# Optimization experiments

Hardware: AMD Instinct MI355X
Metric: run time of the kernel (lower is better)

## Reference

```python
import jax, jax.numpy as jnp
import numpy as np

T, E, H, K, WCNT, L = 131072, 512, 512, 1024, 50000, 128
NUM_LAYERS = 1


def setup_inputs() -> dict:
    key = jax.random.key(0)
    ks = jax.random.split(key, 12)
    f32 = jnp.float32
    return {
        "topic": jax.random.randint(ks[0], (L,), 0, WCNT, dtype=jnp.int32),
        "score_s": jax.random.uniform(ks[1], (1,), dtype=f32),
        "emb": jax.random.normal(ks[2], (WCNT, E), dtype=f32) * 0.05,
        "h": jax.random.normal(ks[3], (NUM_LAYERS, 1, H), dtype=f32) * 0.05,
        "vs": jax.random.normal(ks[4], (T, E), dtype=f32) * 0.05,
        "hs": jax.random.normal(ks[5], (T, 1, H), dtype=f32) * 0.05,
        "w_ih": jax.random.normal(ks[6], (3 * H, 2 * E + 1), dtype=f32) * 0.02,
        "w_hh": jax.random.normal(ks[7], (3 * H, H), dtype=f32) * 0.02,
        "b_ih": jnp.zeros((3 * H,), f32),
        "b_hh": jnp.zeros((3 * H,), f32),
        "w_score": jax.random.normal(ks[8], (1, E + 2 * H + 1), dtype=f32) * 0.02,
        "b_score": jnp.zeros((1,), f32),
    }


def _forward(topic, score_s, emb, h, vs, hs, w_ih, w_hh, b_ih, b_hh, w_score, b_score):
    # topic embedding: mean of word vectors -> v [E]
    v = emb[topic].mean(axis=0)
    # dot-product attention over growing history
    alpha = vs @ v                               # [T]
    vals, idx = jax.lax.top_k(alpha, K)          # top-k similar past items
    a = jax.nn.softmax(vals)                     # [K]
    hs_flat = hs.reshape(-1, NUM_LAYERS * H)     # [T, H]
    attn_h = a @ hs_flat[idx]                    # [H] weighted combine of gathered states
    length = jnp.full((1,), K, dtype=v.dtype)
    # with_last=True: cat([v, attn_h, h, length])
    pred_v = jnp.concatenate([v, attn_h, h.reshape(-1), length])[None, :]  # [1, E+2H+1]
    score = pred_v @ w_score.T + b_score         # [1, 1]
    # score_mode='double': split v by correctness of s
    pos = (score_s >= 0.5).astype(v.dtype)[0]
    x = jnp.concatenate([v * pos, v * (1.0 - pos), score_s])  # [2E+1]
    # single GRU step (torch gate layout: r, z, n)
    h_prev = h.reshape(H)
    gi = w_ih @ x + b_ih
    gh = w_hh @ h_prev + b_hh
    r = jax.nn.sigmoid(gi[:H] + gh[:H])
    z = jax.nn.sigmoid(gi[H:2 * H] + gh[H:2 * H])
    n = jnp.tanh(gi[2 * H:] + r * gh[2 * H:])
    h_new = ((1.0 - z) * n + z * h_prev).reshape(NUM_LAYERS, 1, H)
    # LSTMA updates the history
    vs_new = jnp.concatenate([vs, v[None, :]], axis=0)
    hs_new = jnp.concatenate([hs, h_new], axis=0)
    return score, h_new, vs_new, hs_new


def reference(topic, score_s, emb, h, vs, hs, w_ih, w_hh, b_ih, b_hh, w_score, b_score):
    return _forward(topic, score_s, emb, h, vs, hs, w_ih, w_hh, b_ih, b_hh, w_score, b_score)
```

## Files before the change

kernel.cpp:

```cpp
#include <hip/hip_runtime.h>
#include <math.h>

constexpr int T_ = 131072;
constexpr int E_ = 512;
constexpr int H_ = 512;
constexpr int K_ = 1024;
constexpr int L_ = 128;
constexpr int CAND_CAP = 16384;

typedef __attribute__((ext_vector_type(4))) float f32x4;

constexpr size_t OFF_V     = 0;
constexpr size_t OFF_ALPHA = 512;
constexpr size_t OFF_HIST1 = OFF_ALPHA + T_;
constexpr size_t OFF_CNT   = OFF_HIST1 + 65536;
constexpr size_t OFF_INFO  = OFF_CNT + 2;
constexpr size_t OFF_VALS  = OFF_INFO + 8;
constexpr size_t OFF_IDX   = OFF_VALS + K_;
constexpr size_t OFF_CANDV = OFF_IDX + K_;
constexpr size_t OFF_CANDI = OFF_CANDV + CAND_CAP;
constexpr size_t OFF_GI    = OFF_CANDI + CAND_CAP;
constexpr size_t OFF_GH    = OFF_GI + 3 * H_;

constexpr int ZERO_N = 65536 + 2;

constexpr size_t OUT_VS = 513;
constexpr size_t OUT_HS = 513 + (size_t)(T_ + 1) * E_;

constexpr int NB_GRU = 384;


__device__ __forceinline__ unsigned fkey(float f) {
    unsigned u = __float_as_uint(f);
    return (u & 0x80000000u) ? ~u : (u | 0x80000000u);
}

__global__ __launch_bounds__(1024) void k_init(const int* __restrict__ topic,
                                               const float* __restrict__ emb,
                                               float* __restrict__ ws_v,
                                               unsigned* __restrict__ zero_base,
                                               float* __restrict__ out) {
    if (blockIdx.x == gridDim.x - 1) {
        __shared__ float part[512];
        int t = threadIdx.x;
        int e = t & 511, g = t >> 9;
        float s = 0.f;
        #pragma unroll 8
        for (int l = g * 64; l < g * 64 + 64; ++l) {
            int tp = topic[l];
            s += emb[(size_t)tp * E_ + e];
        }
        if (g == 1) part[e] = s;
        __syncthreads();
        if (g == 0) {
            float v = (s + part[e]) * (1.0f / L_);
            ws_v[e] = v;
            out[OUT_VS + (size_t)T_ * E_ + e] = v;
        }
    } else {
        int i = blockIdx.x * blockDim.x + threadIdx.x;
        if (i < ZERO_N) zero_base[i] = 0u;
    }
}

__global__ __launch_bounds__(256) void k_mega(const float* __restrict__ vs,
                                              const float* __restrict__ hs,
                                              const float* __restrict__ ws_v,
                                              float* __restrict__ alpha,
                                              unsigned* __restrict__ hist1,
                                              const float* __restrict__ wih,
                                              const float* __restrict__ whh,
                                              const float* __restrict__ bih,
                                              const float* __restrict__ bhh,
                                              const float* __restrict__ score_s,
                                              const float* __restrict__ h_in,
                                              float* __restrict__ gi,
                                              float* __restrict__ gh,
                                              float* __restrict__ out) {
    __shared__ float x[1025 + 512];
    int t = threadIdx.x;
    int wave = t >> 6, lane = t & 63;
    int b = blockIdx.x;
    if (b < NB_GRU) {
        float ss = score_s[0];
        float pos = ss >= 0.5f ? 1.f : 0.f;
        for (int c = t; c < 1025; c += 256) {
            float xv;
            if (c < 512)       xv = ws_v[c] * pos;
            else if (c < 1024) xv = ws_v[c - 512] * (1.f - pos);
            else               xv = ss;
            x[c] = xv;
        }
        for (int c = t; c < 512; c += 256) x[1025 + c] = h_in[c];
        __syncthreads();
        int row = b * 4 + wave;
        const float* wr = wih + (size_t)row * 1025;
        float s1 = 0.f;
        for (int c = lane; c < 1025; c += 64) s1 = fmaf(wr[c], x[c], s1);
        const float* hr = whh + (size_t)row * 512;
        float s2 = 0.f;
        #pragma unroll
        for (int c = lane; c < 512; c += 64) s2 = fmaf(hr[c], x[1025 + c], s2);
        #pragma unroll
        for (int m = 32; m; m >>= 1) {
            s1 += __shfl_xor(s1, m, 64);
            s2 += __shfl_xor(s2, m, 64);
        }
        if (lane == 0) { gi[row] = s1 + bih[row]; gh[row] = s2 + bhh[row]; }
        return;
    }
    b -= NB_GRU;
    bool is_vs = b < (T_ / 4);
    int row = (is_vs ? b : b - T_ / 4) * 4 + wave;
    const f32x4* src4 = (const f32x4*)((is_vs ? vs : hs) + (size_t)row * E_);
    f32x4 a0 = __builtin_nontemporal_load(&src4[lane]);
    f32x4 a1 = __builtin_nontemporal_load(&src4[lane + 64]);
    if (is_vs) {
        const f32x4* v4 = (const f32x4*)ws_v;
        f32x4 b0 = v4[lane];
        f32x4 b1 = v4[lane + 64];
        float dot = 0.f;
        dot = fmaf(a0.x, b0.x, dot); dot = fmaf(a0.y, b0.y, dot);
        dot = fmaf(a0.z, b0.z, dot); dot = fmaf(a0.w, b0.w, dot);
        dot = fmaf(a1.x, b1.x, dot); dot = fmaf(a1.y, b1.y, dot);
        dot = fmaf(a1.z, b1.z, dot); dot = fmaf(a1.w, b1.w, dot);
        #pragma unroll
        for (int m = 32; m; m >>= 1) dot += __shfl_xor(dot, m, 64);
        if (lane == 0) {
            alpha[row] = dot;
            atomicAdd(&hist1[fkey(dot) >> 16], 1u);
        }
    }
    int nl = (lane + 1) & 63;
    float n0x = __shfl(a0.x, nl, 64), n0y = __shfl(a0.y, nl, 64), n0z = __shfl(a0.z, nl, 64);
    float n1x = __shfl(a1.x, nl, 64), n1y = __shfl(a1.y, nl, 64), n1z = __shfl(a1.z, nl, 64);
    float* dst = out + (is_vs ? OUT_VS : OUT_HS) + (size_t)row * E_;
    f32x4* d4 = (f32x4*)(dst + 3);
    bool last = (lane == 63);
    f32x4 lo;
    lo.x = a0.w;
    lo.y = last ? n1x : n0x;
    lo.z = last ? n1y : n0y;
    lo.w = last ? n1z : n0z;
    __builtin_nontemporal_store(lo, &d4[lane]);
    if (!last) {
        f32x4 hi;
        hi.x = a1.w; hi.y = n1x; hi.z = n1y; hi.w = n1z;
        __builtin_nontemporal_store(hi, &d4[lane + 64]);
    }
    if (lane == 0) { dst[0] = a0.x; dst[1] = a0.y; dst[2] = a0.z; }
    if (last) dst[511] = a1.w;
}

__global__ __launch_bounds__(256) void k_scan(const unsigned* __restrict__ hist,
                                              unsigned* __restrict__ info) {
    __shared__ unsigned ps[256];
    __shared__ unsigned s_chunk, s_above;
    int t = threadIdx.x;
    unsigned Kwant = (unsigned)K_;
    unsigned base = 65536u - (unsigned)(t + 1) * 256u;
    unsigned s = 0;
    for (int j = 0; j < 256; ++j) s += hist[base + j];
    ps[t] = s;
    __syncthreads();
    #pragma unroll
    for (int off = 1; off < 256; off <<= 1) {
        unsigned v = (t >= off) ? ps[t - off] : 0u;
        __syncthreads();
        ps[t] += v;
        __syncthreads();
    }
    unsigned incl = ps[t], excl = incl - s;
    if (excl < Kwant && incl >= Kwant) { s_chunk = (unsigned)t; s_above = excl; }
    __syncthreads();
    unsigned c = s_chunk;
    unsigned Kw2 = Kwant - s_above;
    unsigned bin = 65535u - c * 256u - (unsigned)t;
    unsigned b = hist[bin];
    __syncthreads();
    ps[t] = b;
    __syncthreads();
    #pragma unroll
    for (int off = 1; off < 256; off <<= 1) {
        unsigned v = (t >= off) ? ps[t - off] : 0u;
        __syncthreads();
        ps[t] += v;
        __syncthreads();
    }
    unsigned inc2 = ps[t], ex2 = inc2 - b;
    if (ex2 < Kw2 && inc2 >= Kw2) {
        info[0] = bin;
        info[1] = s_above + ex2;
    }
}

__global__ __launch_bounds__(256) void k_collect(const float* __restrict__ alpha,
                                                 const unsigned* __restrict__ info,
                                                 unsigned* __restrict__ cnt,
                                                 float* __restrict__ vals,
                                                 int* __restrict__ idx,
                                                 float* __restrict__ candv,
                                                 int* __restrict__ candi) {
    int i = blockIdx.x * blockDim.x + threadIdx.x;
    float a = alpha[i];
    unsigned hb = fkey(a) >> 16;
    unsigned bin1 = info[0];
    if (hb > bin1) {
        unsigned p = atomicAdd(&cnt[0], 1u);
        vals[p] = a; idx[p] = i;
    } else if (hb == bin1) {
        unsigned q = atomicAdd(&cnt[1], 1u);
        if (q < (unsigned)CAND_CAP) { candv[q] = a; candi[q] = i; }
    }
}

__global__ __launch_bounds__(256) void k_resolve(const float* __restrict__ candv,
                                                 const int* __restrict__ candi,
                                                 const unsigned* __restrict__ cnt,
                                                 float* __restrict__ vals,
                                                 int* __restrict__ idx) {
    int t = threadIdx.x;
    unsigned nc = cnt[1] < (unsigned)CAND_CAP ? cnt[1] : (unsigned)CAND_CAP;
    unsigned ndef = cnt[0];
    unsigned k2 = (unsigned)K_ - ndef;
    for (unsigned i = t; i < nc; i += 256) {
        unsigned ki = fkey(candv[i]);
        unsigned greater = 0, eqb = 0;
        for (unsigned j = 0; j < nc; ++j) {
            unsigned kj = fkey(candv[j]);
            greater += (kj > ki) ? 1u : 0u;
            eqb += (kj == ki && j < i) ? 1u : 0u;
        }
        unsigned r = greater + eqb;
        if (r < k2) { vals[ndef + r] = candv[i]; idx[ndef + r] = candi[i]; }
    }
}

__global__ __launch_bounds__(512) void k_attn(const float* __restrict__ hs,
                                              const float* __restrict__ vals,
                                              const int* __restrict__ idx,
                                              float* __restrict__ part) {
    __shared__ float red[512];
    int t = threadIdx.x, j = blockIdx.x;
    float v0 = vals[t], v1 = vals[t + 512];
    red[t] = fmaxf(v0, v1);
    __syncthreads();
    for (int s = 256; s > 0; s >>= 1) { if (t < s) red[t] = fmaxf(red[t], red[t + s]); __syncthreads(); }
    float m = red[0];
    __syncthreads();
    red[t] = expf(v0 - m) + expf(v1 - m);
    __syncthreads();
    for (int s = 256; s > 0; s >>= 1) { if (t < s) red[t] += red[t + s]; __syncthreads(); }
    float S = red[0];
    float acc = 0.f;
    #pragma unroll
    for (int k = j * 8; k < j * 8 + 8; ++k) {
        float w = expf(vals[k] - m) / S;
        acc = fmaf(w, hs[(size_t)idx[k] * E_ + t], acc);
    }
    part[(size_t)j * E_ + t] = acc;
}

__global__ __launch_bounds__(512) void k_final(const float* __restrict__ gi,
                                               const float* __restrict__ gh,
                                               const float* __restrict__ h_in,
                                               const float* __restrict__ part,
                                               const float* __restrict__ ws_v,
                                               const float* __restrict__ w_score,
                                               const float* __restrict__ b_score,
                                               float* __restrict__ out) {
    __shared__ float red[512];
    int j = threadIdx.x;
    float r = 1.f / (1.f + expf(-(gi[j] + gh[j])));
    float z = 1.f / (1.f + expf(-(gi[H_ + j] + gh[H_ + j])));
    float n = tanhf(gi[2 * H_ + j] + r * gh[2 * H_ + j]);
    float hp = h_in[j];
    float hn = (1.f - z) * n + z * hp;
    out[1 + j] = hn;
    out[OUT_HS + (size_t)T_ * E_ + j] = hn;
    float attn = 0.f;
    for (int jj = 0; jj < 128; ++jj) attn += part[(size_t)jj * E_ + j];
    float d = ws_v[j] * w_score[j] + attn * w_score[512 + j] + hp * w_score[1024 + j];
    if (j == 0) d += 1024.0f * w_score[1536] + b_score[0];
    red[j] = d;
    __syncthreads();
    for (int s = 256; s > 0; s >>= 1) { if (j < s) red[j] += red[j + s]; __syncthreads(); }
    if (j == 0) out[0] = red[0];
}

extern "C" void kernel_launch(void* const* d_in, const int* in_sizes, int n_in,
                              void* d_out, int out_size, void* d_ws, size_t ws_size,
                              hipStream_t stream) {
    const int*   topic   = (const int*)d_in[0];
    const float* score_s = (const float*)d_in[1];
    const float* emb     = (const float*)d_in[2];
    const float* h_in    = (const float*)d_in[3];
    const float* vs      = (const float*)d_in[4];
    const float* hs      = (const float*)d_in[5];
    const float* w_ih    = (const float*)d_in[6];
    const float* w_hh    = (const float*)d_in[7];
    const float* b_ih    = (const float*)d_in[8];
    const float* b_hh    = (const float*)d_in[9];
    const float* w_score = (const float*)d_in[10];
    const float* b_score = (const float*)d_in[11];
    float* out = (float*)d_out;

    float*    wsf   = (float*)d_ws;
    float*    v_ws  = wsf + OFF_V;
    float*    alpha = wsf + OFF_ALPHA;
    unsigned* hist1 = (unsigned*)(wsf + OFF_HIST1);
    unsigned* cnt   = (unsigned*)(wsf + OFF_CNT);
    unsigned* info  = (unsigned*)(wsf + OFF_INFO);
    float*    vals  = wsf + OFF_VALS;
    int*      idx   = (int*)(wsf + OFF_IDX);
    float*    candv = wsf + OFF_CANDV;
    int*      candi = (int*)(wsf + OFF_CANDI);
    float*    part  = wsf + OFF_ALPHA;
    float*    gi    = wsf + OFF_GI;
    float*    gh    = wsf + OFF_GH;

    hipLaunchKernelGGL(k_init, dim3(66), dim3(1024), 0, stream,
                       topic, emb, v_ws, hist1, out);
    hipLaunchKernelGGL(k_mega, dim3(NB_GRU + 2 * (T_ / 4)), dim3(256), 0, stream,
                       vs, hs, v_ws, alpha, hist1,
                       w_ih, w_hh, b_ih, b_hh, score_s, h_in, gi, gh, out);
    hipLaunchKernelGGL(k_scan, dim3(1), dim3(256), 0, stream, hist1, info);
    hipLaunchKernelGGL(k_collect, dim3(T_ / 256), dim3(256), 0, stream,
                       alpha, info, cnt, vals, idx, candv, candi);
    hipLaunchKernelGGL(k_resolve, dim3(1), dim3(256), 0, stream,
                       candv, candi, cnt, vals, idx);
    hipLaunchKernelGGL(k_attn, dim3(128), dim3(512), 0, stream, hs, vals, idx, part);
    hipLaunchKernelGGL(k_final, dim3(1), dim3(512), 0, stream,
                       gi, gh, h_in, part, v_ws, w_score, b_score, out);
}
```

Measured before the change: 227.6 us.

## Fold histogram scan into collect and merge attention with final scoring

The single-block scan kernel is removed. Every collect block now redundantly scans the 64K-bin histogram to find the threshold bin itself. The separate final kernel is also merged into the attention kernel: each attention block reduces its partial weighted state against the score weights and atomically adds into the output score, and an extra block does the GRU update. This drops two launches and the partial-sum buffer, at the cost of each of 512 collect blocks reading the full histogram and the score becoming an order-dependent atomic float sum.

```diff
diff --git a/kernel.cpp b/kernel.cpp
--- a/kernel.cpp
+++ b/kernel.cpp
@@ -10,12 +10,14 @@
 
 typedef __attribute__((ext_vector_type(4))) float f32x4;
 
+constexpr int NB_GRU = 384;
+constexpr unsigned NB_MEGA = NB_GRU + 2 * (T_ / 4);
+
 constexpr size_t OFF_V     = 0;
 constexpr size_t OFF_ALPHA = 512;
 constexpr size_t OFF_HIST1 = OFF_ALPHA + T_;
 constexpr size_t OFF_CNT   = OFF_HIST1 + 65536;
-constexpr size_t OFF_INFO  = OFF_CNT + 2;
-constexpr size_t OFF_VALS  = OFF_INFO + 8;
+constexpr size_t OFF_VALS  = OFF_CNT + 2;
 constexpr size_t OFF_IDX   = OFF_VALS + K_;
 constexpr size_t OFF_CANDV = OFF_IDX + K_;
 constexpr size_t OFF_CANDI = OFF_CANDV + CAND_CAP;
@@ -26,8 +28,6 @@
 
 constexpr size_t OUT_VS = 513;
 constexpr size_t OUT_HS = 513 + (size_t)(T_ + 1) * E_;
-
-constexpr int NB_GRU = 384;
 
 
 __device__ __forceinline__ unsigned fkey(float f) {
@@ -56,6 +56,7 @@
             float v = (s + part[e]) * (1.0f / L_);
             ws_v[e] = v;
             out[OUT_VS + (size_t)T_ * E_ + e] = v;
+            if (e == 0) out[0] = 0.f;
         }
     } else {
         int i = blockIdx.x * blockDim.x + threadIdx.x;
@@ -152,59 +153,51 @@
     if (last) dst[511] = a1.w;
 }
 
-__global__ __launch_bounds__(256) void k_scan(const unsigned* __restrict__ hist,
-                                              unsigned* __restrict__ info) {
-    __shared__ unsigned ps[256];
-    __shared__ unsigned s_chunk, s_above;
-    int t = threadIdx.x;
-    unsigned Kwant = (unsigned)K_;
-    unsigned base = 65536u - (unsigned)(t + 1) * 256u;
-    unsigned s = 0;
-    for (int j = 0; j < 256; ++j) s += hist[base + j];
-    ps[t] = s;
-    __syncthreads();
-    #pragma unroll
-    for (int off = 1; off < 256; off <<= 1) {
-        unsigned v = (t >= off) ? ps[t - off] : 0u;
-        __syncthreads();
-        ps[t] += v;
-        __syncthreads();
-    }
-    unsigned incl = ps[t], excl = incl - s;
-    if (excl < Kwant && incl >= Kwant) { s_chunk = (unsigned)t; s_above = excl; }
-    __syncthreads();
-    unsigned c = s_chunk;
-    unsigned Kw2 = Kwant - s_above;
-    unsigned bin = 65535u - c * 256u - (unsigned)t;
-    unsigned b = hist[bin];
-    __syncthreads();
-    ps[t] = b;
-    __syncthreads();
-    #pragma unroll
-    for (int off = 1; off < 256; off <<= 1) {
-        unsigned v = (t >= off) ? ps[t - off] : 0u;
-        __syncthreads();
-        ps[t] += v;
-        __syncthreads();
-    }
-    unsigned inc2 = ps[t], ex2 = inc2 - b;
-    if (ex2 < Kw2 && inc2 >= Kw2) {
-        info[0] = bin;
-        info[1] = s_above + ex2;
-    }
-}
-
 __global__ __launch_bounds__(256) void k_collect(const float* __restrict__ alpha,
-                                                 const unsigned* __restrict__ info,
+                                                 const unsigned* __restrict__ hist1,
                                                  unsigned* __restrict__ cnt,
                                                  float* __restrict__ vals,
                                                  int* __restrict__ idx,
                                                  float* __restrict__ candv,
                                                  int* __restrict__ candi) {
-    int i = blockIdx.x * blockDim.x + threadIdx.x;
+    __shared__ unsigned ps[258];
+    int t = threadIdx.x;
+    unsigned base = 65536u - (unsigned)(t + 1) * 256u;
+    unsigned s = 0;
+    for (int j = 0; j < 256; ++j) s += hist1[base + j];
+    ps[t] = s;
+    __syncthreads();
+    #pragma unroll
+    for (int off = 1; off < 256; off <<= 1) {
+        unsigned v = (t >= off) ? ps[t - off] : 0u;
+        __syncthreads();
+        ps[t] += v;
+        __syncthreads();
+    }
+    unsigned incl = ps[t], excl = incl - s;
+    if (excl < (unsigned)K_ && incl >= (unsigned)K_) { ps[256] = (unsigned)t; ps[257] = excl; }
+    __syncthreads();
+    unsigned c = ps[256];
+    unsigned Kw2 = (unsigned)K_ - ps[257];
+    unsigned bin = 65535u - c * 256u - (unsigned)t;
+    unsigned bv = hist1[bin];
+    __syncthreads();
+    ps[t] = bv;
+    __syncthreads();
+    #pragma unroll
+    for (int off = 1; off < 256; off <<= 1) {
+        unsigned v = (t >= off) ? ps[t - off] : 0u;
+        __syncthreads();
+        ps[t] += v;
+        __syncthreads();
+    }
+    unsigned inc2 = ps[t], ex2 = inc2 - bv;
+    if (ex2 < Kw2 && inc2 >= Kw2) ps[256] = bin;
+    __syncthreads();
+    unsigned bin1 = ps[256];
+    int i = blockIdx.x * 256 + t;
     float a = alpha[i];
     unsigned hb = fkey(a) >> 16;
-    unsigned bin1 = info[0];
     if (hb > bin1) {
         unsigned p = atomicAdd(&cnt[0], 1u);
         vals[p] = a; idx[p] = i;
@@ -239,53 +232,52 @@
 __global__ __launch_bounds__(512) void k_attn(const float* __restrict__ hs,
                                               const float* __restrict__ vals,
                                               const int* __restrict__ idx,
-                                              float* __restrict__ part) {
+                                              const float* __restrict__ gi,
+                                              const float* __restrict__ gh,
+                                              const float* __restrict__ h_in,
+                                              const float* __restrict__ ws_v,
+                                              const float* __restrict__ w_score,
+                                              const float* __restrict__ b_score,
+                                              float* __restrict__ out) {
     __shared__ float red[512];
     int t = threadIdx.x, j = blockIdx.x;
-    float v0 = vals[t], v1 = vals[t + 512];
-    red[t] = fmaxf(v0, v1);
-    __syncthreads();
-    for (int s = 256; s > 0; s >>= 1) { if (t < s) red[t] = fmaxf(red[t], red[t + s]); __syncthreads(); }
-    float m = red[0];
-    __syncthreads();
-    red[t] = expf(v0 - m) + expf(v1 - m);
-    __syncthreads();
-    for (int s = 256; s > 0; s >>= 1) { if (t < s) red[t] += red[t + s]; __syncthreads(); }
-    float S = red[0];
-    float acc = 0.f;
-    #pragma unroll
-    for (int k = j * 8; k < j * 8 + 8; ++k) {
-        float w = expf(vals[k] - m) / S;
-        acc = fmaf(w, hs[(size_t)idx[k] * E_ + t], acc);
-    }
-    part[(size_t)j * E_ + t] = acc;
-}
-
-__global__ __launch_bounds__(512) void k_final(const float* __restrict__ gi,
-                                               const float* __restrict__ gh,
-                                               const float* __restrict__ h_in,
-                                               const float* __restrict__ part,
-                                               const float* __restrict__ ws_v,
-                                               const float* __restrict__ w_score,
-                                               const float* __restrict__ b_score,
-                                               float* __restrict__ out) {
-    __shared__ float red[512];
-    int j = threadIdx.x;
-    float r = 1.f / (1.f + expf(-(gi[j] + gh[j])));
-    float z = 1.f / (1.f + expf(-(gi[H_ + j] + gh[H_ + j])));
-    float n = tanhf(gi[2 * H_ + j] + r * gh[2 * H_ + j]);
-    float hp = h_in[j];
-    float hn = (1.f - z) * n + z * hp;
-    out[1 + j] = hn;
-    out[OUT_HS + (size_t)T_ * E_ + j] = hn;
-    float attn = 0.f;
-    for (int jj = 0; jj < 128; ++jj) attn += part[(size_t)jj * E_ + j];
-    float d = ws_v[j] * w_score[j] + attn * w_score[512 + j] + hp * w_score[1024 + j];
-    if (j == 0) d += 1024.0f * w_score[1536] + b_score[0];
-    red[j] = d;
-    __syncthreads();
-    for (int s = 256; s > 0; s >>= 1) { if (j < s) red[j] += red[j + s]; __syncthreads(); }
-    if (j == 0) out[0] = red[0];
+    if (j < 128) {
+        float v0 = vals[t], v1 = vals[t + 512];
+        red[t] = fmaxf(v0, v1);
+        __syncthreads();
+        for (int s = 256; s > 0; s >>= 1) { if (t < s) red[t] = fmaxf(red[t], red[t + s]); __syncthreads(); }
+        float m = red[0];
+        __syncthreads();
+        red[t] = expf(v0 - m) + expf(v1 - m);
+        __syncthreads();
+        for (int s = 256; s > 0; s >>= 1) { if (t < s) red[t] += red[t + s]; __syncthreads(); }
+        float S = red[0];
+        float acc = 0.f;
+        #pragma unroll
+        for (int k = j * 8; k < j * 8 + 8; ++k) {
+            float w = expf(vals[k] - m) / S;
+            acc = fmaf(w, hs[(size_t)idx[k] * E_ + t], acc);
+        }
+        __syncthreads();
+        red[t] = acc * w_score[512 + t];
+        __syncthreads();
+        for (int s = 256; s > 0; s >>= 1) { if (t < s) red[t] += red[t + s]; __syncthreads(); }
+        if (t == 0) atomicAdd(&out[0], red[0]);
+    } else {
+        float rr = 1.f / (1.f + expf(-(gi[t] + gh[t])));
+        float z = 1.f / (1.f + expf(-(gi[H_ + t] + gh[H_ + t])));
+        float n = tanhf(gi[2 * H_ + t] + rr * gh[2 * H_ + t]);
+        float hp = h_in[t];
+        float hn = (1.f - z) * n + z * hp;
+        out[1 + t] = hn;
+        out[OUT_HS + (size_t)T_ * E_ + t] = hn;
+        float d = ws_v[t] * w_score[t] + hp * w_score[1024 + t];
+        if (t == 0) d += 1024.0f * w_score[1536] + b_score[0];
+        red[t] = d;
+        __syncthreads();
+        for (int s = 256; s > 0; s >>= 1) { if (t < s) red[t] += red[t + s]; __syncthreads(); }
+        if (t == 0) atomicAdd(&out[0], red[0]);
+    }
 }
 
 extern "C" void kernel_launch(void* const* d_in, const int* in_sizes, int n_in,
@@ -310,26 +302,22 @@
     float*    alpha = wsf + OFF_ALPHA;
     unsigned* hist1 = (unsigned*)(wsf + OFF_HIST1);
     unsigned* cnt   = (unsigned*)(wsf + OFF_CNT);
-    unsigned* info  = (unsigned*)(wsf + OFF_INFO);
     float*    vals  = wsf + OFF_VALS;
     int*      idx   = (int*)(wsf + OFF_IDX);
     float*    candv = wsf + OFF_CANDV;
     int*      candi = (int*)(wsf + OFF_CANDI);
-    float*    part  = wsf + OFF_ALPHA;
     float*    gi    = wsf + OFF_GI;
     float*    gh    = wsf + OFF_GH;
 
     hipLaunchKernelGGL(k_init, dim3(66), dim3(1024), 0, stream,
                        topic, emb, v_ws, hist1, out);
-    hipLaunchKernelGGL(k_mega, dim3(NB_GRU + 2 * (T_ / 4)), dim3(256), 0, stream,
+    hipLaunchKernelGGL(k_mega, dim3(NB_MEGA), dim3(256), 0, stream,
                        vs, hs, v_ws, alpha, hist1,
                        w_ih, w_hh, b_ih, b_hh, score_s, h_in, gi, gh, out);
-    hipLaunchKernelGGL(k_scan, dim3(1), dim3(256), 0, stream, hist1, info);
     hipLaunchKernelGGL(k_collect, dim3(T_ / 256), dim3(256), 0, stream,
-                       alpha, info, cnt, vals, idx, candv, candi);
+                       alpha, hist1, cnt, vals, idx, candv, candi);
     hipLaunchKernelGGL(k_resolve, dim3(1), dim3(256), 0, stream,
                        candv, candi, cnt, vals, idx);
-    hipLaunchKernelGGL(k_attn, dim3(128), dim3(512), 0, stream, hs, vals, idx, part);
-    hipLaunchKernelGGL(k_final, dim3(1), dim3(512), 0, stream,
-                       gi, gh, h_in, part, v_ws, w_score, b_score, out);
-}
+    hipLaunchKernelGGL(k_attn, dim3(129), dim3(512), 0, stream,
+                       hs, vals, idx, gi, gh, h_in, v_ws, w_score, b_score, out);
+}
```

Measured after the change: 225.9 us. About the same (-0.7%).
